# Optimization experiments

Measured on AMD Instinct MI355X. Metric: run time of the kernel, lower is better.

Reference implementation:

```python
import jax, jax.numpy as jnp
import numpy as np

N = 8192            # number of ROIs
FEAT = 255          # num_classes(151) + embed_dim(100) + pos_dim(4)
HID = 64
PRE_NMS = 6000      # eval-mode pre_nms_topn
POST_NMS = 300      # eval-mode post_nms_topn
NMS_THRESH = 0.7


def setup_inputs() -> dict:
    key = jax.random.key(0)
    ks = jax.random.split(key, 12)
    # rois: [N,5] = (im_ind, x1, y1, x2, y2), valid boxes in a 1024x1024 image
    x1 = jax.random.uniform(ks[0], (N,)) * 900.0
    y1 = jax.random.uniform(ks[1], (N,)) * 900.0
    w = jax.random.uniform(ks[2], (N,)) * 120.0 + 4.0
    h = jax.random.uniform(ks[3], (N,)) * 120.0 + 4.0
    rois = jnp.stack([jnp.zeros((N,)), x1, y1, x1 + w, y1 + h], axis=1).astype(jnp.float32)
    roi_feat = jax.random.normal(ks[4], (N, FEAT), dtype=jnp.float32)
    s = 0.05
    return {
        "rois": rois,
        "roi_feat": roi_feat,
        "W_sub1": jax.random.normal(ks[5], (FEAT, HID), jnp.float32) * s,
        "b_sub1": jnp.zeros((HID,), jnp.float32),
        "W_sub2": jax.random.normal(ks[6], (HID, HID), jnp.float32) * s,
        "b_sub2": jnp.zeros((HID,), jnp.float32),
        "W_obj1": jax.random.normal(ks[7], (FEAT, HID), jnp.float32) * s,
        "b_obj1": jnp.zeros((HID,), jnp.float32),
        "W_obj2": jax.random.normal(ks[8], (HID, HID), jnp.float32) * s,
        "b_obj2": jnp.zeros((HID,), jnp.float32),
    }


def _iou_matrix(boxes):
    # boxes: [K,4] (x1,y1,x2,y2) -> [K,K] IoU
    x1, y1, x2, y2 = boxes[:, 0], boxes[:, 1], boxes[:, 2], boxes[:, 3]
    area = (x2 - x1) * (y2 - y1)
    ix1 = jnp.maximum(x1[:, None], x1[None, :])
    iy1 = jnp.maximum(y1[:, None], y1[None, :])
    ix2 = jnp.minimum(x2[:, None], x2[None, :])
    iy2 = jnp.minimum(y2[:, None], y2[None, :])
    inter = jnp.maximum(ix2 - ix1, 0.0) * jnp.maximum(iy2 - iy1, 0.0)
    return inter / (area[:, None] + area[None, :] - inter + 1e-8)


def reference(rois, roi_feat, W_sub1, b_sub1, W_sub2, b_sub2,
              W_obj1, b_obj1, W_obj2, b_obj2):
    # Original detaches roi_feat before the bilinear head.
    f = jax.lax.stop_gradient(roi_feat)
    x_sub = jnp.maximum(f @ W_sub1 + b_sub1, 0.0) @ W_sub2 + b_sub2  # [N,64]
    x_obj = jnp.maximum(f @ W_obj1 + b_obj1, 0.0) @ W_obj2 + b_obj2  # [N,64]
    scores = jax.nn.sigmoid(x_sub @ x_obj.T)                          # [N,N]

    n = scores.shape[0]
    # exclude self-pairs (sub == obj)
    diag = jnp.arange(n)
    flat = scores.at[diag, diag].set(-1.0).reshape(-1)

    # pre-NMS top-k over all N*N pairs (sorted descending)
    top_s, top_i = jax.lax.top_k(flat, PRE_NMS)
    sub = top_i // n
    obj = top_i % n

    boxes = jax.lax.stop_gradient(rois[:, 1:5])
    bs, bo = boxes[sub], boxes[obj]
    # union box of each (sub,obj) pair for relation NMS
    union = jnp.concatenate([jnp.minimum(bs[:, :2], bo[:, :2]),
                             jnp.maximum(bs[:, 2:], bo[:, 2:])], axis=1)  # [PRE,4]
    iou = _iou_matrix(union)                                              # [PRE,PRE]
    # non-greedy (matrix) NMS: suppress i if any higher-ranked j overlaps > thresh
    higher = jnp.triu(jnp.ones((PRE_NMS, PRE_NMS), bool), k=1)  # [j,i] true when j < i
    suppressed = jnp.any((iou > NMS_THRESH) & higher, axis=0)
    kept_scores = jnp.where(suppressed, -1.0, top_s)

    post_s, post_k = jax.lax.top_k(kept_scores, POST_NMS)
    rel_inds = jnp.stack([sub[post_k], obj[post_k]], axis=1)  # [POST,2]
    return rel_inds, post_s
```

## Files before the change

### kernel.cpp

```cpp
#include <hip/hip_runtime.h>
#include <math.h>

#define NB    8192
#define FEAT  255
#define HID   64
#define TOPK  6000
#define POSTK 300
#define BINS  8192
#define BSHIFT 19
#define CAP   131072
#define CAPLIM 49152
#define SLACK 1
#define TSEL  1000
#define JSLICES 128
#define LCAP  2048
#define NMS_ICH 64

typedef __attribute__((ext_vector_type(8))) short bf16x8;
typedef __attribute__((ext_vector_type(4))) float f32x4;
typedef __attribute__((ext_vector_type(4))) double f64x4;

__device__ __forceinline__ unsigned binOf(float x) {
    unsigned u = __float_as_uint(x);
    u = (u & 0x80000000u) ? ~u : (u | 0x80000000u);
    return u >> BSHIFT;
}

__device__ __forceinline__ unsigned short f2bf(float f) {
    unsigned u = __float_as_uint(f);
    return (unsigned short)((u + 0x7fffu + ((u >> 16) & 1u)) >> 16);
}

__global__ __launch_bounds__(256) void mlp_kernel(
    const float* __restrict__ feat,
    const float* __restrict__ W1s, const float* __restrict__ b1s,
    const float* __restrict__ W2s, const float* __restrict__ b2s,
    const float* __restrict__ W1o, const float* __restrict__ b1o,
    const float* __restrict__ W2o, const float* __restrict__ b2o,
    double* __restrict__ Xs64, double* __restrict__ Xo64,
    unsigned short* __restrict__ Xsb, unsigned short* __restrict__ Xob)
{
    __shared__ float  fl[16 * 258];
    __shared__ double hl[2][16][65];

    int tid  = threadIdx.x;
    int lane = tid & 63;
    int w    = tid >> 6;
    int a16  = lane & 15;
    int kq   = lane >> 4;
    int net  = w & 1;
    int p    = w >> 1;
    int rbase = blockIdx.x * 16;

    const float* fsrc = feat + (size_t)rbase * FEAT;
    for (int idx = tid; idx < 16 * FEAT; idx += 256) {
        int r = idx / FEAT;
        int k = idx - r * FEAT;
        fl[r * 258 + k] = fsrc[idx];
    }
    if (tid < 16) fl[tid * 258 + 255] = 0.0f;
    __syncthreads();

    const float* W1 = net ? W1o : W1s;
    const float* B1 = net ? b1o : b1s;
    const float* W2 = net ? W2o : W2s;
    const float* B2 = net ? b2o : b2s;
    double*       X  = net ? Xo64 : Xs64;
    unsigned short* Xb = net ? Xob : Xsb;

    int c0 = (2 * p) * 16 + a16;
    int c1 = (2 * p + 1) * 16 + a16;

    f64x4 acc0 = {0, 0, 0, 0}, acc1 = {0, 0, 0, 0};
#pragma unroll 4
    for (int ks = 0; ks < 63; ++ks) {
        int k = ks * 4 + kq;
        double av = (double)fl[a16 * 258 + k];
        double b0 = (double)W1[k * HID + c0];
        double b1 = (double)W1[k * HID + c1];
        acc0 = __builtin_amdgcn_mfma_f64_16x16x4f64(av, b0, acc0, 0, 0, 0);
        acc1 = __builtin_amdgcn_mfma_f64_16x16x4f64(av, b1, acc1, 0, 0, 0);
    }
    {
        int k = 252 + kq;
        double av = (double)fl[a16 * 258 + k];
        double b0 = 0.0, b1 = 0.0;
        if (k < FEAT) {
            b0 = (double)W1[k * HID + c0];
            b1 = (double)W1[k * HID + c1];
        }
        acc0 = __builtin_amdgcn_mfma_f64_16x16x4f64(av, b0, acc0, 0, 0, 0);
        acc1 = __builtin_amdgcn_mfma_f64_16x16x4f64(av, b1, acc1, 0, 0, 0);
    }

    {
        double bb0 = (double)B1[c0], bb1 = (double)B1[c1];
#pragma unroll
        for (int i = 0; i < 4; ++i) {
            int r = kq * 4 + i;
            double v0 = acc0[i] + bb0;
            double v1 = acc1[i] + bb1;
            hl[net][r][c0] = v0 > 0.0 ? v0 : 0.0;
            hl[net][r][c1] = v1 > 0.0 ? v1 : 0.0;
        }
    }
    __syncthreads();

    f64x4 x0 = {0, 0, 0, 0}, x1 = {0, 0, 0, 0};
#pragma unroll 4
    for (int ks = 0; ks < 16; ++ks) {
        int k = ks * 4 + kq;
        double av = hl[net][a16][k];
        double b0 = (double)W2[k * HID + c0];
        double b1 = (double)W2[k * HID + c1];
        x0 = __builtin_amdgcn_mfma_f64_16x16x4f64(av, b0, x0, 0, 0, 0);
        x1 = __builtin_amdgcn_mfma_f64_16x16x4f64(av, b1, x1, 0, 0, 0);
    }

    {
        double bb0 = (double)B2[c0], bb1 = (double)B2[c1];
#pragma unroll
        for (int i = 0; i < 4; ++i) {
            int r = kq * 4 + i;
            double v0 = x0[i] + bb0;
            double v1 = x1[i] + bb1;
            size_t o0 = (size_t)(rbase + r) * HID + c0;
            size_t o1 = (size_t)(rbase + r) * HID + c1;
            X[o0] = v0; X[o1] = v1;
            Xb[o0] = f2bf((float)v0);
            Xb[o1] = f2bf((float)v1);
        }
    }
}

__global__ __launch_bounds__(256) void mfma_hist(
    const unsigned short* __restrict__ Xsb, const unsigned short* __restrict__ Xob,
    unsigned* __restrict__ ghist)
{
    __shared__ unsigned hist[BINS];
    int tid = threadIdx.x;
    for (int i = tid; i < BINS; i += 256) hist[i] = 0u;
    __syncthreads();

    int lane = tid & 63;
    int wave = tid >> 6;
    int quad = lane >> 4;
    int l16  = lane & 15;
    int r0 = blockIdx.y * 128 + (wave >> 1) * 64;
    int c0 = blockIdx.x * 128 + (wave & 1) * 64;

    f32x4 acc[4][4];
    bf16x8 afr[2][4], bfr[2][4];
#pragma unroll
    for (int kc = 0; kc < 2; ++kc)
#pragma unroll
        for (int t = 0; t < 4; ++t) {
            afr[kc][t] = *(const bf16x8*)(Xsb + (size_t)(r0 + t * 16 + l16) * HID + kc * 32 + quad * 8);
            bfr[kc][t] = *(const bf16x8*)(Xob + (size_t)(c0 + t * 16 + l16) * HID + kc * 32 + quad * 8);
        }
#pragma unroll
    for (int ti = 0; ti < 4; ++ti)
#pragma unroll
        for (int tj = 0; tj < 4; ++tj) acc[ti][tj] = (f32x4){0, 0, 0, 0};
#pragma unroll
    for (int kc = 0; kc < 2; ++kc)
#pragma unroll
        for (int ti = 0; ti < 4; ++ti)
#pragma unroll
            for (int tj = 0; tj < 4; ++tj)
                acc[ti][tj] = __builtin_amdgcn_mfma_f32_16x16x32_bf16(
                    afr[kc][ti], bfr[kc][tj], acc[ti][tj], 0, 0, 0);

#pragma unroll
    for (int ti = 0; ti < 4; ++ti)
#pragma unroll
        for (int tj = 0; tj < 4; ++tj)
#pragma unroll
            for (int i = 0; i < 4; ++i) {
                int r = r0 + ti * 16 + quad * 4 + i;
                int c = c0 + tj * 16 + l16;
                float v = acc[ti][tj][i];
                if (v > 0.0f && r != c)
                    atomicAdd(&hist[binOf(v)], 1u);
            }

    __syncthreads();
    for (int i = tid; i < BINS; i += 256) {
        unsigned h = hist[i];
        if (h) atomicAdd(&ghist[i], h);
    }
}

__global__ __launch_bounds__(256) void find_threshold(
    const unsigned* __restrict__ ghist, unsigned* __restrict__ ctrl)
{
    __shared__ unsigned csum[256];
    int tid  = threadIdx.x;
    int base = tid * (BINS / 256);
    unsigned s = 0;
    for (int i = 0; i < BINS / 256; ++i) s += ghist[base + i];
    csum[tid] = s;
    __syncthreads();
    if (tid == 0) {
        unsigned run = 0;
        for (int c = 255; c >= 0; --c) { run += csum[c]; csum[c] = run; }
    }
    __syncthreads();

    unsigned above = (tid == 255) ? 0u : csum[tid + 1];
    unsigned prev = above;
    for (int b = base + BINS / 256 - 1; b >= base; --b) {
        unsigned cur = prev + ghist[b];
        if (cur >= TSEL && prev < TSEL) {
            unsigned bstar = (unsigned)b;
            unsigned bt = bstar >= SLACK ? bstar - SLACK : 0;
            unsigned cnt = cur;
            for (unsigned bb = bstar; bb-- > bt;) cnt += ghist[bb];
            while (8u * cnt > CAPLIM && bt < bstar) { cnt -= ghist[bt]; bt++; }
            ctrl[1] = bt;
            unsigned key = bt << BSHIFT;
            unsigned fbits;
            if (key == 0u) fbits = 0xff800000u;
            else fbits = (key & 0x80000000u) ? (key ^ 0x80000000u) : ~key;
            ctrl[2] = fbits;
            break;
        }
        prev = cur;
    }
}

__global__ __launch_bounds__(256) void mfma_filter(
    const unsigned short* __restrict__ Xsb, const unsigned short* __restrict__ Xob,
    unsigned* __restrict__ ctrl, unsigned* __restrict__ cidx)
{
    __shared__ unsigned lcnt;
    __shared__ unsigned gbase;
    __shared__ unsigned lbuf[LCAP];
    float vt = __uint_as_float(ctrl[2]);
    int tid = threadIdx.x;
    if (tid == 0) lcnt = 0;

    int lane = tid & 63;
    int wave = tid >> 6;
    int quad = lane >> 4;
    int l16  = lane & 15;
    int r0 = blockIdx.y * 128 + (wave >> 1) * 64;
    int cb = blockIdx.x * 256 + (wave & 1) * 64;

    bf16x8 afr[2][4];
#pragma unroll
    for (int kc = 0; kc < 2; ++kc)
#pragma unroll
        for (int t = 0; t < 4; ++t)
            afr[kc][t] = *(const bf16x8*)(Xsb + (size_t)(r0 + t * 16 + l16) * HID + kc * 32 + quad * 8);

    bf16x8 b0[2], b1[2];
    {
        int col0 = cb + l16;
        int col1 = cb + 16 + l16;
#pragma unroll
        for (int kc = 0; kc < 2; ++kc) {
            b0[kc] = *(const bf16x8*)(Xob + (size_t)col0 * HID + kc * 32 + quad * 8);
            b1[kc] = *(const bf16x8*)(Xob + (size_t)col1 * HID + kc * 32 + quad * 8);
        }
    }

    __syncthreads();

#pragma unroll
    for (int q = 0; q < 8; ++q) {
        int ct = q >> 2, tj = q & 3;
        int c0 = cb + ct * 128;
        int cj = c0 + tj * 16 + l16;
        bool nodiag = (r0 != c0);

        bf16x8 b2[2];
        if (q < 6) {
            int q2 = q + 2;
            int col2 = cb + (q2 >> 2) * 128 + (q2 & 3) * 16 + l16;
#pragma unroll
            for (int kc = 0; kc < 2; ++kc)
                b2[kc] = *(const bf16x8*)(Xob + (size_t)col2 * HID + kc * 32 + quad * 8);
        }

        f32x4 acc[4];
#pragma unroll
        for (int ti = 0; ti < 4; ++ti) acc[ti] = (f32x4){0, 0, 0, 0};
#pragma unroll
        for (int kc = 0; kc < 2; ++kc)
#pragma unroll
            for (int ti = 0; ti < 4; ++ti)
                acc[ti] = __builtin_amdgcn_mfma_f32_16x16x32_bf16(
                    afr[kc][ti], b0[kc], acc[ti], 0, 0, 0);

        if (nodiag) {
#pragma unroll
            for (int ti = 0; ti < 4; ++ti)
#pragma unroll
                for (int i = 0; i < 4; ++i) {
                    if (acc[ti][i] >= vt) {
                        int r = r0 + ti * 16 + quad * 4 + i;
                        unsigned rc = (unsigned)r * (unsigned)NB + (unsigned)cj;
                        unsigned p = atomicAdd(&lcnt, 1u);
                        if (p < LCAP) {
                            lbuf[p] = rc;
                        } else {
                            unsigned g = atomicAdd(&ctrl[0], 1u);
                            if (g < CAP) cidx[g] = rc;
                        }
                    }
                }
        } else {
#pragma unroll
            for (int ti = 0; ti < 4; ++ti)
#pragma unroll
                for (int i = 0; i < 4; ++i) {
                    int r = r0 + ti * 16 + quad * 4 + i;
                    if (acc[ti][i] >= vt && r != cj) {
                        unsigned rc = (unsigned)r * (unsigned)NB + (unsigned)cj;
                        unsigned p = atomicAdd(&lcnt, 1u);
                        if (p < LCAP) {
                            lbuf[p] = rc;
                        } else {
                            unsigned g = atomicAdd(&ctrl[0], 1u);
                            if (g < CAP) cidx[g] = rc;
                        }
                    }
                }
        }

        if (q < 6) {
            b0[0] = b1[0]; b0[1] = b1[1];
            b1[0] = b2[0]; b1[1] = b2[1];
        } else if (q == 6) {
            b0[0] = b1[0]; b0[1] = b1[1];
        }
    }

    __syncthreads();
    unsigned n = lcnt; if (n > LCAP) n = LCAP;
    if (tid == 0 && n) gbase = atomicAdd(&ctrl[0], n);
    __syncthreads();
    for (unsigned i = tid; i < n; i += 256u) {
        unsigned p = gbase + i;
        if (p < CAP) cidx[p] = lbuf[i];
    }
}

__global__ __launch_bounds__(256) void refine_kernel(
    const unsigned* __restrict__ ctrl, const unsigned* __restrict__ cidx,
    const double* __restrict__ Xs64, const double* __restrict__ Xo64,
    double* __restrict__ cval)
{
    unsigned M = ctrl[0];
    if (M > CAP) M = CAP;
    unsigned nw = gridDim.x * 4u;
    int lane = threadIdx.x & 63;
    for (unsigned w = blockIdx.x * 4u + (threadIdx.x >> 6); w < M; w += nw) {
        unsigned id = cidx[w];
        unsigned r = id >> 13, c = id & (NB - 1);
        double p = Xs64[(size_t)r * HID + lane] * Xo64[(size_t)c * HID + lane];
#pragma unroll
        for (int s = 32; s > 0; s >>= 1) p += __shfl_xor(p, s);
        if (lane == 0) cval[w] = (r == c) ? -1.0 : p;
    }
}

__global__ __launch_bounds__(256) void rank_count(
    const unsigned* __restrict__ ctrl,
    const double* __restrict__ cval, const unsigned* __restrict__ cidx,
    unsigned* __restrict__ rank)
{
    unsigned M = ctrl[0];
    if (M > CAP) M = CAP;

    unsigned slice = blockIdx.y;
    unsigned jbeg = (unsigned)(((unsigned long long)slice * M) / JSLICES);
    unsigned jend = (unsigned)(((unsigned long long)(slice + 1) * M) / JSLICES);

    __shared__ double  lv[256];
    __shared__ unsigned li[256];

    for (unsigned itile = blockIdx.x; itile * 1024u < M; itile += gridDim.x) {
        unsigned i0 = itile * 1024u + threadIdx.x;
        double v[4];
        unsigned id[4];
        unsigned cnt[4] = {0, 0, 0, 0};
#pragma unroll
        for (int k = 0; k < 4; ++k) {
            unsigned idx = i0 + (unsigned)k * 256u;
            bool a = idx < M;
            v[k]  = a ? cval[idx] : 0.0;
            id[k] = a ? cidx[idx] : 0u;
        }

        for (unsigned base = jbeg; base < jend; base += 256u) {
            unsigned j = base + threadIdx.x;
            if (j < jend) { lv[threadIdx.x] = cval[j]; li[threadIdx.x] = cidx[j]; }
            __syncthreads();
            unsigned lim = jend - base; if (lim > 256u) lim = 256u;
            for (unsigned e = 0; e < lim; ++e) {
                double ev = lv[e];
                unsigned ei = li[e];
#pragma unroll
                for (int k = 0; k < 4; ++k)
                    cnt[k] += (ev > v[k]) || (ev == v[k] && ei < id[k]);
            }
            __syncthreads();
        }
#pragma unroll
        for (int k = 0; k < 4; ++k) {
            unsigned idx = i0 + (unsigned)k * 256u;
            if (idx < M && cnt[k]) atomicAdd(&rank[idx], cnt[k]);
        }
    }
}

__global__ __launch_bounds__(256) void rank_scatter_prep(
    const unsigned* __restrict__ ctrl,
    const double* __restrict__ cval, const unsigned* __restrict__ cidx,
    const unsigned* __restrict__ rank, const float* __restrict__ rois,
    double* __restrict__ sval, unsigned* __restrict__ sidx,
    double* __restrict__ ub)
{
    unsigned M = ctrl[0];
    if (M > CAP) M = CAP;
    unsigned stride = gridDim.x * 256u;
    for (unsigned t = blockIdx.x * 256u + threadIdx.x; t < M; t += stride) {
        unsigned rk = rank[t];
        if (rk < TOPK) {
            unsigned id = cidx[t];
            sval[rk] = cval[t];
            sidx[rk] = id;
            unsigned s = id >> 13, o = id & (NB - 1);
            const float* bs = rois + (size_t)s * 5;
            const float* bo = rois + (size_t)o * 5;
            double x1 = fmin((double)bs[1], (double)bo[1]);
            double y1 = fmin((double)bs[2], (double)bo[2]);
            double x2 = fmax((double)bs[3], (double)bo[3]);
            double y2 = fmax((double)bs[4], (double)bo[4]);
            double area = (x2 - x1) * (y2 - y1);
            double* u = ub + (size_t)rk * 5;
            u[0] = x1; u[1] = y1; u[2] = x2; u[3] = y2; u[4] = 0.7 * area;
        }
    }
}

__global__ __launch_bounds__(256) void nms_kernel(
    const double* __restrict__ ub, unsigned* sup)
{
    int jb = blockIdx.x;
    int ic = blockIdx.y;
    int ibase = ic * NMS_ICH;
    if (ibase >= TOPK) return;
    if (ibase >= jb * 256 + 255) return;

    __shared__ double L[NMS_ICH][5];
    int tid = threadIdx.x;
    int icount = TOPK - ibase; if (icount > NMS_ICH) icount = NMS_ICH;
    for (int q = tid; q < icount * 5; q += 256)
        L[q / 5][q % 5] = ub[(size_t)ibase * 5 + q];
    __syncthreads();

    int j = jb * 256 + tid;
    if (j >= TOPK) return;
    int lim = j - ibase; if (lim > icount) lim = icount;
    if (lim <= 0) return;

    const double* u = ub + (size_t)j * 5;
    double x1 = u[0], y1 = u[1], x2 = u[2], y2 = u[3], pa = u[4];
    bool flag = false;
    for (int e = 0; e < lim; ++e) {
        double ix1 = fmax(L[e][0], x1);
        double iy1 = fmax(L[e][1], y1);
        double ix2 = fmin(L[e][2], x2);
        double iy2 = fmin(L[e][3], y2);
        double iw = ix2 - ix1; iw = iw > 0.0 ? iw : 0.0;
        double ih = iy2 - iy1; ih = ih > 0.0 ? ih : 0.0;
        flag |= (1.7 * (iw * ih) > pa + L[e][4] + 7e-9);
    }
    if (flag) sup[j] = 1u;
}

__global__ __launch_bounds__(1024) void finalize_kernel(
    const unsigned* __restrict__ sup, const double* __restrict__ sval,
    const unsigned* __restrict__ sidx, float* __restrict__ out)
{
    __shared__ unsigned wsum[16];
    __shared__ unsigned red[16];
    __shared__ unsigned bases[2];
    __shared__ unsigned totalu_s;
    int tid  = threadIdx.x;
    int lane = tid & 63;
    int w    = tid >> 6;

    unsigned s = 0;
    for (int i = tid; i < TOPK; i += 1024) s += (sup[i] == 0u);
#pragma unroll
    for (int st = 32; st > 0; st >>= 1) s += __shfl_down(s, st);
    if (lane == 0) red[w] = s;
    __syncthreads();
    if (tid == 0) {
        unsigned tot = 0;
        for (int i = 0; i < 16; ++i) tot += red[i];
        totalu_s = tot; bases[0] = 0; bases[1] = 0;
    }
    __syncthreads();
    unsigned totalu = totalu_s;

    for (int c = 0; c < (TOPK + 1023) / 1024; ++c) {
        int idx = c * 1024 + tid;
        int valid = TOPK - c * 1024; if (valid > 1024) valid = 1024;
        unsigned f = (idx < TOPK && sup[idx] == 0u) ? 1u : 0u;
        unsigned long long m = __ballot(f != 0u);
        if (lane == 0) wsum[w] = (unsigned)__popcll(m);
        __syncthreads();
        unsigned wbase = 0, ctot = 0;
        for (int i = 0; i < 16; ++i) {
            unsigned v = wsum[i];
            if (i < w) wbase += v;
            ctot += v;
        }
        unsigned e = wbase + (unsigned)__popcll(m & ((1ull << lane) - 1ull));
        if (idx < TOPK) {
            unsigned pos = f ? (bases[0] + e)
                             : (totalu + bases[1] + (unsigned)tid - e);
            if (pos < POSTK) {
                unsigned id = sidx[idx];
                unsigned sb = id >> 13, ob = id & (NB - 1);
                out[2 * pos]     = (float)sb;
                out[2 * pos + 1] = (float)ob;
                double sg = f ? 1.0 / (1.0 + exp(-sval[idx])) : -1.0;
                out[2 * POSTK + pos] = (float)sg;
            }
        }
        __syncthreads();
        if (tid == 0) {
            bases[0] += ctot;
            bases[1] += (unsigned)valid - ctot;
        }
        __syncthreads();
    }
}

extern "C" void kernel_launch(void* const* d_in, const int* in_sizes, int n_in,
                              void* d_out, int out_size, void* d_ws, size_t ws_size,
                              hipStream_t stream)
{
    const float* rois = (const float*)d_in[0];
    const float* feat = (const float*)d_in[1];
    const float* W1s  = (const float*)d_in[2];
    const float* b1s  = (const float*)d_in[3];
    const float* W2s  = (const float*)d_in[4];
    const float* b2s  = (const float*)d_in[5];
    const float* W1o  = (const float*)d_in[6];
    const float* b1o  = (const float*)d_in[7];
    const float* W2o  = (const float*)d_in[8];
    const float* b2o  = (const float*)d_in[9];

    char* ws = (char*)d_ws;
    size_t off = 0;
    auto alloc = [&](size_t bytes) -> void* {
        off = (off + 255) & ~(size_t)255;
        void* p = ws + off;
        off += bytes;
        return p;
    };

    unsigned* ghist = (unsigned*)alloc((size_t)BINS * 4);
    unsigned* ctrl  = (unsigned*)alloc(256);
    unsigned* sup   = (unsigned*)alloc((size_t)6144 * 4);
    unsigned* rank  = (unsigned*)alloc((size_t)CAP * 4);
    size_t zero_bytes = off;

    double* Xs64 = (double*)alloc((size_t)NB * HID * 8);
    double* Xo64 = (double*)alloc((size_t)NB * HID * 8);
    unsigned short* Xsb = (unsigned short*)alloc((size_t)NB * HID * 2);
    unsigned short* Xob = (unsigned short*)alloc((size_t)NB * HID * 2);
    double* cval = (double*)alloc((size_t)CAP * 8);
    unsigned* cidx = (unsigned*)alloc((size_t)CAP * 4);
    double* svalv = (double*)alloc((size_t)TOPK * 8);
    unsigned* sidxv = (unsigned*)alloc((size_t)TOPK * 4);
    double* ub   = (double*)alloc((size_t)TOPK * 5 * 8);

    hipMemsetAsync(d_ws, 0, zero_bytes, stream);

    mlp_kernel<<<NB / 16, 256, 0, stream>>>(feat, W1s, b1s, W2s, b2s,
                                            W1o, b1o, W2o, b2o,
                                            Xs64, Xo64, Xsb, Xob);
    mfma_hist<<<dim3(8, 64), 256, 0, stream>>>(Xsb, Xob, ghist);
    find_threshold<<<1, 256, 0, stream>>>(ghist, ctrl);
    mfma_filter<<<dim3(32, 64), 256, 0, stream>>>(Xsb, Xob, ctrl, cidx);
    refine_kernel<<<2048, 256, 0, stream>>>(ctrl, cidx, Xs64, Xo64, cval);
    rank_count<<<dim3(16, JSLICES), 256, 0, stream>>>(ctrl, cval, cidx, rank);
    rank_scatter_prep<<<512, 256, 0, stream>>>(ctrl, cval, cidx, rank, rois,
                                               svalv, sidxv, ub);
    nms_kernel<<<dim3((TOPK + 255) / 256, (TOPK + NMS_ICH - 1) / NMS_ICH), 256, 0, stream>>>(ub, sup);
    finalize_kernel<<<1, 1024, 0, stream>>>(sup, svalv, sidxv, (float*)d_out);
}
```

Before: 227.8 us.

## Fuse threshold search into sampled histogram kernel and add wave-level hit skip

The histogram kernel now covers half as many columns (grid 4x64 instead of 8x64), so it is a sparser sample of the score matrix. TSEL is halved and the capacity check uses a sample factor of 16 to match. The separate find_threshold launch is folded into the histogram kernel: the last block to finish, found with an atomic counter, reads the global histogram and computes the threshold. In the filter kernel, hits are gathered into a bitmask and the atomic-append path is skipped when no lane in the wave has a hit. The risk is that a coarser sample gives a less accurate threshold, which could let the candidate count overflow or fall short.

```diff
diff --git a/kernel.cpp b/kernel.cpp
--- a/kernel.cpp
+++ b/kernel.cpp
@@ -11,7 +11,8 @@
 #define CAP   131072
 #define CAPLIM 49152
 #define SLACK 1
-#define TSEL  1000
+#define TSEL  500
+#define SAMPF 16
 #define JSLICES 128
 #define LCAP  2048
 #define NMS_ICH 64
@@ -135,9 +136,11 @@
 
 __global__ __launch_bounds__(256) void mfma_hist(
     const unsigned short* __restrict__ Xsb, const unsigned short* __restrict__ Xob,
-    unsigned* __restrict__ ghist)
+    unsigned* __restrict__ ghist, unsigned* __restrict__ ctrl)
 {
     __shared__ unsigned hist[BINS];
+    __shared__ unsigned csum[256];
+    __shared__ bool win_s;
     int tid = threadIdx.x;
     for (int i = tid; i < BINS; i += 256) hist[i] = 0u;
     __syncthreads();
@@ -189,16 +192,23 @@
         unsigned h = hist[i];
         if (h) atomicAdd(&ghist[i], h);
     }
-}
-
-__global__ __launch_bounds__(256) void find_threshold(
-    const unsigned* __restrict__ ghist, unsigned* __restrict__ ctrl)
-{
-    __shared__ unsigned csum[256];
-    int tid  = threadIdx.x;
+
+    __syncthreads();
+    if (tid == 0) {
+        __threadfence();
+        unsigned done = atomicAdd(&ctrl[3], 1u);
+        win_s = (done == gridDim.x * gridDim.y - 1u);
+    }
+    __syncthreads();
+    if (!win_s) return;
+
+    for (int i = tid; i < BINS; i += 256)
+        hist[i] = __hip_atomic_load(&ghist[i], __ATOMIC_RELAXED, __HIP_MEMORY_SCOPE_AGENT);
+    __syncthreads();
+
     int base = tid * (BINS / 256);
     unsigned s = 0;
-    for (int i = 0; i < BINS / 256; ++i) s += ghist[base + i];
+    for (int i = 0; i < BINS / 256; ++i) s += hist[base + i];
     csum[tid] = s;
     __syncthreads();
     if (tid == 0) {
@@ -210,13 +220,13 @@
     unsigned above = (tid == 255) ? 0u : csum[tid + 1];
     unsigned prev = above;
     for (int b = base + BINS / 256 - 1; b >= base; --b) {
-        unsigned cur = prev + ghist[b];
+        unsigned cur = prev + hist[b];
         if (cur >= TSEL && prev < TSEL) {
             unsigned bstar = (unsigned)b;
             unsigned bt = bstar >= SLACK ? bstar - SLACK : 0;
             unsigned cnt = cur;
-            for (unsigned bb = bstar; bb-- > bt;) cnt += ghist[bb];
-            while (8u * cnt > CAPLIM && bt < bstar) { cnt -= ghist[bt]; bt++; }
+            for (unsigned bb = bstar; bb-- > bt;) cnt += hist[bb];
+            while ((unsigned)SAMPF * cnt > CAPLIM && bt < bstar) { cnt -= hist[bt]; bt++; }
             ctrl[1] = bt;
             unsigned key = bt << BSHIFT;
             unsigned fbits;
@@ -293,30 +303,26 @@
                 acc[ti] = __builtin_amdgcn_mfma_f32_16x16x32_bf16(
                     afr[kc][ti], b0[kc], acc[ti], 0, 0, 0);
 
-        if (nodiag) {
+        unsigned hm = 0u;
+#pragma unroll
+        for (int ti = 0; ti < 4; ++ti)
+#pragma unroll
+            for (int i = 0; i < 4; ++i) {
+                bool hit = acc[ti][i] >= vt;
+                if (!nodiag) {
+                    int r = r0 + ti * 16 + quad * 4 + i;
+                    hit = hit && (r != cj);
+                }
+                hm |= hit ? (1u << (ti * 4 + i)) : 0u;
+            }
+
+        if (__any(hm != 0u)) {
 #pragma unroll
             for (int ti = 0; ti < 4; ++ti)
 #pragma unroll
                 for (int i = 0; i < 4; ++i) {
-                    if (acc[ti][i] >= vt) {
+                    if (hm & (1u << (ti * 4 + i))) {
                         int r = r0 + ti * 16 + quad * 4 + i;
-                        unsigned rc = (unsigned)r * (unsigned)NB + (unsigned)cj;
-                        unsigned p = atomicAdd(&lcnt, 1u);
-                        if (p < LCAP) {
-                            lbuf[p] = rc;
-                        } else {
-                            unsigned g = atomicAdd(&ctrl[0], 1u);
-                            if (g < CAP) cidx[g] = rc;
-                        }
-                    }
-                }
-        } else {
-#pragma unroll
-            for (int ti = 0; ti < 4; ++ti)
-#pragma unroll
-                for (int i = 0; i < 4; ++i) {
-                    int r = r0 + ti * 16 + quad * 4 + i;
-                    if (acc[ti][i] >= vt && r != cj) {
                         unsigned rc = (unsigned)r * (unsigned)NB + (unsigned)cj;
                         unsigned p = atomicAdd(&lcnt, 1u);
                         if (p < LCAP) {
@@ -588,8 +594,7 @@
     mlp_kernel<<<NB / 16, 256, 0, stream>>>(feat, W1s, b1s, W2s, b2s,
                                             W1o, b1o, W2o, b2o,
                                             Xs64, Xo64, Xsb, Xob);
-    mfma_hist<<<dim3(8, 64), 256, 0, stream>>>(Xsb, Xob, ghist);
-    find_threshold<<<1, 256, 0, stream>>>(ghist, ctrl);
+    mfma_hist<<<dim3(4, 64), 256, 0, stream>>>(Xsb, Xob, ghist, ctrl);
     mfma_filter<<<dim3(32, 64), 256, 0, stream>>>(Xsb, Xob, ctrl, cidx);
     refine_kernel<<<2048, 256, 0, stream>>>(ctrl, cidx, Xs64, Xo64, cval);
     rank_count<<<dim3(16, JSLICES), 256, 0, stream>>>(ctrl, cval, cidx, rank);
```

New measurement: 225.3 us. About the same (-1.1%).
